# Optimization experiments

Hardware: AMD Instinct MI355X
Metric: run time of the kernel (lower is better)

Reference implementation:

```python
import jax, jax.numpy as jnp
import numpy as np

STRIDES = (8, 16, 32, 64, 128)
SIZES = (128, 64, 32, 16, 8)
B, C = 16, 80
K = 1000            # pre_nms_max_boxes
THRESHOLD = 0.05    # detection confidence threshold
NMS_THR = 0.5
PAD = -1.0


def setup_inputs() -> dict:
    key = jax.random.key(0)
    ks = jax.random.split(key, 15)
    inp = {}
    for i, (s, hw) in enumerate(zip(STRIDES, SIZES)):
        inp[f"cls{i}"] = jax.random.normal(ks[3 * i], (B, C, hw, hw), jnp.float32)
        # reg is post-ReLU (non-negative) distances; scale by stride for realistic extents
        inp[f"reg{i}"] = jax.random.uniform(ks[3 * i + 1], (B, 4, hw, hw), jnp.float32) * (2.0 * s)
        inp[f"ctr{i}"] = jax.random.normal(ks[3 * i + 2], (B, 1, hw, hw), jnp.float32)
    return inp


def _decode_level(cls_l, ctr_l, reg_l, stride):
    # cls_l: [B,C,H,W] logits, ctr_l: [B,1,H,W] logits, reg_l: [B,4,H,W] (l,t,r,b)
    b, c, h, w = cls_l.shape
    p = jax.nn.sigmoid(cls_l)
    cen = jax.nn.sigmoid(ctr_l)
    scaled = jnp.sqrt(p * cen)  # sqrt(cls * centerness), broadcast over C
    ys = jnp.arange(h, dtype=cls_l.dtype) * stride + stride / 2.0
    xs = jnp.arange(w, dtype=cls_l.dtype) * stride + stride / 2.0
    cx = jnp.broadcast_to(xs[None, :], (h, w))
    cy = jnp.broadcast_to(ys[:, None], (h, w))
    l, t, r, bt = reg_l[:, 0], reg_l[:, 1], reg_l[:, 2], reg_l[:, 3]  # [B,H,W]
    boxes = jnp.stack([cx - l, cy - t, cx + r, cy + bt], axis=-1)  # [B,H,W,4]
    return p.reshape(b, c, h * w), scaled.reshape(b, c, h * w), boxes.reshape(b, h * w, 4)


def _iou_matrix(boxes):
    # boxes: [K,4] -> [K,K] IoU
    x1, y1, x2, y2 = boxes[:, 0], boxes[:, 1], boxes[:, 2], boxes[:, 3]
    area = jnp.clip(x2 - x1, 0.0) * jnp.clip(y2 - y1, 0.0)
    ix1 = jnp.maximum(x1[:, None], x1[None, :])
    iy1 = jnp.maximum(y1[:, None], y1[None, :])
    ix2 = jnp.minimum(x2[:, None], x2[None, :])
    iy2 = jnp.minimum(y2[:, None], y2[None, :])
    inter = jnp.clip(ix2 - ix1, 0.0) * jnp.clip(iy2 - iy1, 0.0)
    union = area[:, None] + area[None, :] - inter
    return inter / jnp.maximum(union, 1e-9)


def _nms_one(boxes, cls_id, valid):
    # greedy class-aware NMS on score-descending boxes; returns keep mask [K]
    iou = _iou_matrix(boxes)
    same = cls_id[:, None] == cls_id[None, :]  # batched_nms: only same class suppresses
    sup = (iou > NMS_THR) & same
    rng = jnp.arange(boxes.shape[0])
    def body(i, keep):
        s = sup[i] & (rng > i) & keep[i]
        return keep & (~s)
    return jax.lax.fori_loop(0, boxes.shape[0], body, valid)


def reference(cls0, cls1, cls2, cls3, cls4,
              reg0, reg1, reg2, reg3, reg4,
              ctr0, ctr1, ctr2, ctr3, ctr4):
    cls_levels = (cls0, cls1, cls2, cls3, cls4)
    reg_levels = (reg0, reg1, reg2, reg3, reg4)
    ctr_levels = (ctr0, ctr1, ctr2, ctr3, ctr4)
    raws, scaleds, boxes_list = [], [], []
    for cl, ct, rg, s in zip(cls_levels, ctr_levels, reg_levels, STRIDES):
        r, sc, bx = _decode_level(cl, ct, rg, s)
        raws.append(r); scaleds.append(sc); boxes_list.append(bx)
    raw = jnp.concatenate(raws, axis=-1)        # [B,C,L]
    scaled = jnp.concatenate(scaleds, axis=-1)  # [B,C,L]
    boxes = jnp.concatenate(boxes_list, axis=1) # [B,L,4]
    b, c, L = raw.shape
    valid = raw >= THRESHOLD  # threshold on raw cls probability
    masked = jnp.where(valid, scaled, -1.0).reshape(b, c * L)
    topv, topi = jax.lax.top_k(masked, K)  # per-batch pre-NMS limit, sorted desc by scaled score
    cls_id = topi // L
    loc = topi % L
    boxes_k = jnp.take_along_axis(boxes, loc[..., None], axis=1)  # [B,K,4]
    scaled_k = jnp.take_along_axis(scaled.reshape(b, c * L), topi, axis=1)  # [B,K]
    valid_k = topv >= 0.0
    keep = jax.vmap(_nms_one)(boxes_k, cls_id, valid_k)  # [B,K]
    out = jnp.concatenate(
        [boxes_k, scaled_k[..., None], cls_id.astype(boxes_k.dtype)[..., None]], axis=-1)  # [B,K,6]
    return jnp.where(keep[..., None], out, PAD)
```

## Files before the change

kernel.cpp:

```cpp
#include <hip/hip_runtime.h>
#include <stdint.h>

typedef uint32_t u32;
typedef uint64_t u64;
typedef unsigned short u16;

#define NB 16
#define NC 80
#define LTOT 21824
#define TOPK 1000
#define CAP2 6144
#define NBINS 1024
#define KEYSH 12
#define BINBASE 0x3F580u
#define T2SQ 0.7119140625f
#define PACKS8 2728
#define CGRP 20
#define NSHARD 8
#define PSH 4096
#define SSTAGE 512

struct P5 { const float* a; const float* b; const float* c; const float* d; const float* e; };

__device__ __forceinline__ const float* selp(const P5& p, int lvl) {
    const float* q = p.a;
    if (lvl == 1) q = p.b;
    else if (lvl == 2) q = p.c;
    else if (lvl == 3) q = p.d;
    else if (lvl == 4) q = p.e;
    return q;
}

__device__ __forceinline__ void locate(int loc, int& lvl, int& off) {
    if (loc < 16384)      { lvl = 0; off = 0; }
    else if (loc < 20480) { lvl = 1; off = 16384; }
    else if (loc < 21504) { lvl = 2; off = 20480; }
    else if (loc < 21760) { lvl = 3; off = 21504; }
    else                  { lvl = 4; off = 21760; }
}

__device__ __forceinline__ void locate_pack8(int pk, int& lvl, int& poff, int& loff) {
    if (pk < 2048)      { lvl = 0; poff = 0;    loff = 0; }
    else if (pk < 2560) { lvl = 1; poff = 2048; loff = 16384; }
    else if (pk < 2688) { lvl = 2; poff = 2560; loff = 20480; }
    else if (pk < 2720) { lvl = 3; poff = 2688; loff = 21504; }
    else                { lvl = 4; poff = 2720; loff = 21760; }
}

__device__ __forceinline__ float sigmoidf_(float x) {
    return 1.0f / (1.0f + expf(-x));
}

__global__ __launch_bounds__(256) void k_ctr(P5 ctr, float* __restrict__ cen, float* __restrict__ Larr,
                                             u32* __restrict__ hist, u32* __restrict__ pcnt,
                                             float* __restrict__ out) {
    int tid = threadIdx.x;
    int b = blockIdx.y;
    if (blockIdx.x == 0) {
        for (int i = tid; i < NBINS; i += 256) hist[b * NBINS + i] = 0;
        if (tid < NSHARD * 16) pcnt[b * NSHARD * 16 + tid] = 0;
    }
    {
        int oi = blockIdx.x * 256 + tid;
        if (oi < TOPK * 6) out[b * TOPK * 6 + oi] = -1.0f;
    }
    int loc = blockIdx.x * 256 + tid;
    if (loc >= LTOT) return;
    int lvl, off; locate(loc, lvl, off);
    int d = loc - off;
    int hw = 1 << (2 * (7 - lvl));
    float x = selp(ctr, lvl)[b * hw + d];
    float cv = sigmoidf_(x);
    float L;
    float q = T2SQ / cv;
    if (!(q < 1.0f)) {
        L = 3.0e38f;
    } else {
        float qm = q * 0.999996f;
        L = logf(qm / (1.0f - qm)) - 1.0e-3f;
    }
    cen[b * LTOT + loc] = cv;
    Larr[b * LTOT + loc] = L;
}

__global__ __launch_bounds__(256, 8) void k_sweep(P5 cls, const float* __restrict__ Larr,
                                                  const float* __restrict__ cen,
                                                  u32* __restrict__ hist, u32* __restrict__ pcnt,
                                                  u64* __restrict__ pcand) {
    __shared__ u32 lh[NBINS];
    __shared__ u64 stage[SSTAGE];
    __shared__ u64 outk[SSTAGE];
    __shared__ u32 scnt, ocnt, sbase;
    int tid = threadIdx.x;
    for (int i = tid; i < NBINS; i += 256) lh[i] = 0;
    if (tid == 0) { scnt = 0; ocnt = 0; }
    __syncthreads();

    int b  = blockIdx.z;
    int cg = blockIdx.y;
    int pk = blockIdx.x * 256 + tid;
    int shard = (blockIdx.x + blockIdx.y) & (NSHARD - 1);
    u32* pc = &pcnt[(b * NSHARD + shard) * 16];
    u64* pdst = pcand + (size_t)(b * NSHARD + shard) * PSH;

    if (pk < PACKS8) {
        int lvl, poff, loff; locate_pack8(pk, lvl, poff, loff);
        int d0 = (pk - poff) * 8;
        int hw = 1 << (2 * (7 - lvl));
        int gl = b * LTOT + loff + d0;
        int loc0 = loff + d0;
        float4 La = *(const float4*)&Larr[gl];
        float4 Lb = *(const float4*)&Larr[gl + 4];
        const float* base = selp(cls, lvl) + ((size_t)(b * NC + cg * 4)) * hw + d0;

        float4 Av[4], Bv[4];
        #pragma unroll
        for (int i = 0; i < 4; ++i) {
            Av[i] = *(const float4*)(base + (size_t)i * hw);
            Bv[i] = *(const float4*)(base + (size_t)i * hw + 4);
        }

        #pragma unroll
        for (int i = 0; i < 4; ++i) {
            float4 a0 = Av[i], b0 = Bv[i];
            bool any = (a0.x >= La.x) | (a0.y >= La.y) | (a0.z >= La.z) | (a0.w >= La.w)
                     | (b0.x >= Lb.x) | (b0.y >= Lb.y) | (b0.z >= Lb.z) | (b0.w >= Lb.w);
            if (any) {
                u32 c = (u32)(cg * 4 + i);
#define ELEM(X, LV, J) \
                if ((X) >= (LV)) { \
                    u32 p = atomicAdd(&scnt, 1u); \
                    u64 ent = ((u64)__float_as_uint(X) << 32) | (u64)((c << 15) | (u32)(loc0 + (J))); \
                    if (p < SSTAGE) stage[p] = ent; \
                    else {  \
                        float cv = cen[gl + (J)]; \
                        float sv = sqrtf(sigmoidf_(X) * cv); \
                        u32 bits = __float_as_uint(sv); \
                        u32 key = bits >> KEYSH; \
                        if (key >= BINBASE) { \
                            atomicAdd(&lh[min(key - BINBASE, (u32)(NBINS - 1))], 1u); \
                            u32 q2 = atomicAdd(pc, 1u); \
                            if (q2 < PSH) pdst[q2] = ((u64)bits << 32) | (u32)(~(c * (u32)LTOT + (u32)(loc0 + (J)))); \
                        } \
                    } \
                }
                ELEM(a0.x, La.x, 0) ELEM(a0.y, La.y, 1) ELEM(a0.z, La.z, 2) ELEM(a0.w, La.w, 3)
                ELEM(b0.x, Lb.x, 4) ELEM(b0.y, Lb.y, 5) ELEM(b0.z, Lb.z, 6) ELEM(b0.w, Lb.w, 7)
#undef ELEM
            }
        }
    }
    __syncthreads();

    u32 m2 = scnt; if (m2 > SSTAGE) m2 = SSTAGE;
    for (u32 i = tid; i < m2; i += 256) {
        u64 e = stage[i];
        u32 xbits = (u32)(e >> 32);
        u32 eid   = (u32)e;
        u32 c     = eid >> 15;
        u32 loc   = eid & 0x7FFFu;
        float X  = __uint_as_float(xbits);
        float cv = cen[b * LTOT + loc];
        float sv = sqrtf(sigmoidf_(X) * cv);
        u32 bits = __float_as_uint(sv);
        u32 key = bits >> KEYSH;
        if (key >= BINBASE) {
            atomicAdd(&lh[min(key - BINBASE, (u32)(NBINS - 1))], 1u);
            u32 p = atomicAdd(&ocnt, 1u);
            outk[p] = ((u64)bits << 32) | (u32)(~(c * (u32)LTOT + loc));
        }
    }
    __syncthreads();

    for (u32 i = tid; i < NBINS; i += 256) {
        u32 v = lh[i];
        if (v) atomicAdd(&hist[b * NBINS + i], v);
    }
    u32 m3 = ocnt; if (m3 > SSTAGE) m3 = SSTAGE;
    if (tid == 0 && m3) sbase = atomicAdd(pc, m3);
    __syncthreads();
    for (u32 i = tid; i < m3; i += 256) {
        u32 q = sbase + i;
        if (q < PSH) pdst[q] = outk[i];
    }
}

__global__ __launch_bounds__(1024) void k_rank(const u64* __restrict__ pcand, const u32* __restrict__ pcnt,
                                               const u32* __restrict__ hist, u32* __restrict__ cnt,
                                               P5 reg, float* __restrict__ boxesWs,
                                               float* __restrict__ scoreWs, int* __restrict__ clsWs) {
    __shared__ u64 sh[CAP2];
    __shared__ u32 tot[NBINS];
    __shared__ u32 sufL[NBINS];
    __shared__ u32 bcnt[NBINS];
    __shared__ u32 wtot[16];
    __shared__ u32 cbase[NSHARD + 1];
    __shared__ u32 thrT;
    int b = blockIdx.x, tid = threadIdx.x;
    int lane = tid & 63, w = tid >> 6;

    u32 v = hist[b * NBINS + tid];
    tot[tid] = v;
    bcnt[tid] = 0;
    if (tid < NSHARD) {
        u32 c0 = pcnt[(b * NSHARD + tid) * 16];
        cbase[tid] = (c0 > (u32)PSH) ? (u32)PSH : c0;
    }
    if (tid == 0) thrT = 0;

    u32 s = v;
    #pragma unroll
    for (int d2 = 1; d2 < 64; d2 <<= 1) {
        u32 t = (u32)__shfl_down((int)s, d2, 64);
        if (lane + d2 < 64) s += t;
    }
    if (lane == 0) wtot[w] = s;
    __syncthreads();

    u32 add = 0;
    #pragma unroll
    for (int w2 = 0; w2 < 16; ++w2) if (w2 > w) add += wtot[w2];
    s += add;
    sufL[tid] = s;
    if (tid == 0) {
        u32 acc = 0;
        #pragma unroll
        for (int i = 0; i < NSHARD; ++i) { u32 t = cbase[i]; cbase[i] = acc; acc += t; }
        cbase[NSHARD] = acc;
    }
    __syncthreads();

    {
        u32 sv = sufL[tid];
        u32 snext = (tid + 1 < NBINS) ? sufL[tid + 1] : 0;
        if (sv >= (u32)TOPK && snext < (u32)TOPK) thrT = (u32)tid;
    }
    __syncthreads();
    u32 T = thrT;
    u32 tb = BINBASE + T;
    u32 totc = cbase[NSHARD];

    for (u32 idx = tid; idx < totc; idx += 1024) {
        int sg = 0;
        #pragma unroll
        for (int i = 1; i < NSHARD; ++i) sg += (idx >= cbase[i]);
        u32 i2 = idx - cbase[sg];
        u64 key = pcand[(size_t)(b * NSHARD + sg) * PSH + i2];
        u32 kb = (u32)(key >> (32 + KEYSH));
        if (kb >= tb) {
            u32 bin = min(kb - BINBASE, (u32)(NBINS - 1));
            u32 pos = (sufL[bin] - tot[bin]) + atomicAdd(&bcnt[bin], 1u);
            if (pos < CAP2) sh[pos] = key;
        }
    }
    __syncthreads();
    u32 n = sufL[T]; if (n > CAP2) n = CAP2;
    if (tid == 0) cnt[b * 16] = (n > (u32)TOPK) ? (u32)TOPK : n;

    for (u32 e = tid; e < n; e += 1024) {
        u64 key = sh[e];
        u32 bin = min((u32)(key >> (32 + KEYSH)) - BINBASE, (u32)(NBINS - 1));
        u32 s0 = sufL[bin] - tot[bin];
        u32 s1 = sufL[bin]; if (s1 > n) s1 = n;
        u32 r = s0;
        for (u32 i2 = s0; i2 < s1; ++i2) r += (sh[i2] > key);
        if (r < TOPK) {
            u32 bits = (u32)(key >> 32);
            u32 idx  = ~((u32)key);
            int c   = (int)(idx / (u32)LTOT);
            int loc = (int)(idx - (u32)c * (u32)LTOT);
            int lvl, off; locate(loc, lvl, off);
            int d = loc - off;
            int logw = 7 - lvl;
            int ww = 1 << logw, hw = ww * ww;
            int y = d >> logw, x = d & (ww - 1);
            const float* rp = selp(reg, lvl);
            int base = (b * 4) * hw + d;
            float lf = rp[base], tf = rp[base + hw], rf = rp[base + 2 * hw], bf = rp[base + 3 * hw];
            int stride = 8 << lvl;
            float cx = (float)(x * stride) + 0.5f * (float)stride;
            float cy = (float)(y * stride) + 0.5f * (float)stride;
            int o = b * TOPK + (int)r;
            boxesWs[o * 4 + 0] = cx - lf; boxesWs[o * 4 + 1] = cy - tf;
            boxesWs[o * 4 + 2] = cx + rf; boxesWs[o * 4 + 3] = cy + bf;
            scoreWs[o] = __uint_as_float(bits); clsWs[o] = c;
        }
    }
}

__global__ __launch_bounds__(64) void k_nms(const float* __restrict__ boxesWs, const float* __restrict__ scoreWs,
                                            const int* __restrict__ clsWs, const u32* __restrict__ cnt,
                                            float* __restrict__ out) {
    __shared__ u16 list[TOPK];
    __shared__ u32 keptW[32];
    int c = blockIdx.x, b = blockIdx.y;
    int lane = threadIdx.x;
    int n = (int)cnt[b * 16]; if (n > TOPK) n = TOPK;

    int m = 0;
    for (int k0 = 0; k0 < n; k0 += 64) {
        int j = k0 + lane;
        int cj = (j < n) ? clsWs[b * TOPK + j] : -2;
        u64 mask = __ballot(cj == c);
        int pos = m + __popcll(mask & ((lane == 0) ? 0ull : (~0ull >> (64 - lane))));
        if (cj == c) list[pos] = (u16)j;
        m += (int)__popcll(mask);
    }
    __syncthreads();
    if (m == 0) return;

    if (m <= 64) {
        int j = (lane < m) ? (int)list[lane] : (int)list[0];
        float4 bx = ((const float4*)boxesWs)[b * TOPK + j];
        float ar = fmaxf(bx.z - bx.x, 0.f) * fmaxf(bx.w - bx.y, 0.f);
        u64 kept = (m < 64) ? ((1ull << m) - 1ull) : ~0ull;
        u64 todo = kept;
        while (todo) {
            int i = __builtin_ctzll(todo);
            todo &= todo - 1;
            float bix = __shfl(bx.x, i, 64);
            float biy = __shfl(bx.y, i, 64);
            float biz = __shfl(bx.z, i, 64);
            float biw = __shfl(bx.w, i, 64);
            float ai  = __shfl(ar,   i, 64);
            float ix1 = fmaxf(bix, bx.x), iy1 = fmaxf(biy, bx.y);
            float ix2 = fminf(biz, bx.z), iy2 = fminf(biw, bx.w);
            float inter = fmaxf(ix2 - ix1, 0.f) * fmaxf(iy2 - iy1, 0.f);
            float uni = fmaxf(ai + ar - inter, 1e-9f);
            float iou = inter / uni;
            u64 sup = __ballot(lane > i && lane < m && iou > 0.5f);
            kept &= ~sup;
            todo &= ~sup;
        }
        if (lane < m && ((kept >> lane) & 1ull)) {
            int o = b * TOPK + j;
            float sc = scoreWs[o];
            out[o * 6 + 0] = bx.x; out[o * 6 + 1] = bx.y; out[o * 6 + 2] = bx.z;
            out[o * 6 + 3] = bx.w; out[o * 6 + 4] = sc;   out[o * 6 + 5] = (float)c;
        }
    } else {
        if (lane < 32) keptW[lane] = 0;
        __syncthreads();
        for (int i = lane; i < m; i += 64) atomicOr(&keptW[i >> 5], 1u << (i & 31));
        __syncthreads();
        for (int i = 0; i < m; ++i) {
            if (!((keptW[i >> 5] >> (i & 31)) & 1u)) { __syncthreads(); continue; }
            int ji = (int)list[i];
            float4 bi = ((const float4*)boxesWs)[b * TOPK + ji];
            float ai = fmaxf(bi.z - bi.x, 0.f) * fmaxf(bi.w - bi.y, 0.f);
            for (int jj = i + 1 + lane; jj < m; jj += 64) {
                int j2 = (int)list[jj];
                float4 bj = ((const float4*)boxesWs)[b * TOPK + j2];
                float aj = fmaxf(bj.z - bj.x, 0.f) * fmaxf(bj.w - bj.y, 0.f);
                float ix1 = fmaxf(bi.x, bj.x), iy1 = fmaxf(bi.y, bj.y);
                float ix2 = fminf(bi.z, bj.z), iy2 = fminf(bi.w, bj.w);
                float inter = fmaxf(ix2 - ix1, 0.f) * fmaxf(iy2 - iy1, 0.f);
                float uni = fmaxf(ai + aj - inter, 1e-9f);
                if (inter / uni > 0.5f) atomicAnd(&keptW[jj >> 5], ~(1u << (jj & 31)));
            }
            __syncthreads();
        }
        for (int i = lane; i < m; i += 64) {
            if ((keptW[i >> 5] >> (i & 31)) & 1u) {
                int j2 = (int)list[i];
                int o = b * TOPK + j2;
                float4 bj = ((const float4*)boxesWs)[o];
                float sc = scoreWs[o];
                out[o * 6 + 0] = bj.x; out[o * 6 + 1] = bj.y; out[o * 6 + 2] = bj.z;
                out[o * 6 + 3] = bj.w; out[o * 6 + 4] = sc;   out[o * 6 + 5] = (float)c;
            }
        }
    }
}

extern "C" void kernel_launch(void* const* d_in, const int* in_sizes, int n_in,
                              void* d_out, int out_size, void* d_ws, size_t ws_size,
                              hipStream_t stream) {
    const float* cls[5]; const float* reg[5]; const float* ctr[5];
    for (int i = 0; i < 5; ++i) {
        cls[i] = (const float*)d_in[3 * i + 0];
        reg[i] = (const float*)d_in[3 * i + 1];
        ctr[i] = (const float*)d_in[3 * i + 2];
    }
    P5 Pc = { cls[0], cls[1], cls[2], cls[3], cls[4] };
    P5 Pr = { reg[0], reg[1], reg[2], reg[3], reg[4] };
    P5 Pt = { ctr[0], ctr[1], ctr[2], ctr[3], ctr[4] };

    char* ws = (char*)d_ws;
    u32*   hist    = (u32*)(ws + 0);
    u32*   pcnt    = (u32*)(ws + 131072);
    u32*   cnt     = (u32*)(ws + 196608);
    float* cen     = (float*)(ws + 262144);
    float* Larr    = (float*)(ws + 1703936);
    u64*   pcand   = (u64*)(ws + 3145728);
    float* boxesWs = (float*)(ws + 7864320);
    float* scoreWs = (float*)(ws + 8388608);
    int*   clsWs   = (int*)(ws + 8519680);

    k_ctr<<<dim3((LTOT + 255) / 256, NB), 256, 0, stream>>>(Pt, cen, Larr, hist, pcnt, (float*)d_out);
    dim3 sweep((PACKS8 + 255) / 256, CGRP, NB);
    k_sweep<<<sweep, 256, 0, stream>>>(Pc, Larr, cen, hist, pcnt, pcand);
    k_rank<<<NB, 1024, 0, stream>>>(pcand, pcnt, hist, cnt, Pr, boxesWs, scoreWs, clsWs);
    k_nms<<<dim3(NC, NB), 64, 0, stream>>>(boxesWs, scoreWs, clsWs, cnt, (float*)d_out);
}
```

Before: 59.46 us.

## Fuse centerness into sweep and merge rank with per-class NMS

The separate centerness kernel goes away: each sweep thread now loads the centerness logits and computes the screening threshold and sigmoid inline, and the zeroing of histogram and counters moves to a memset. The rank and NMS kernels are merged into one block per batch, with boxes, scores and classes kept in shared memory and each of 16 waves handling 5 classes in turn. Every output slot is written exactly once, either as a box or as padding. This removes two launches and the global round-trips through the workspace, at the cost of recomputing sigmoid/log per class group, and it serialises NMS into 16 blocks with one wave per class instead of 1280 blocks.

```diff
diff --git a/kernel.cpp b/kernel.cpp
--- a/kernel.cpp
+++ b/kernel.cpp
@@ -51,44 +51,19 @@
     return 1.0f / (1.0f + expf(-x));
 }
 
-__global__ __launch_bounds__(256) void k_ctr(P5 ctr, float* __restrict__ cen, float* __restrict__ Larr,
-                                             u32* __restrict__ hist, u32* __restrict__ pcnt,
-                                             float* __restrict__ out) {
-    int tid = threadIdx.x;
-    int b = blockIdx.y;
-    if (blockIdx.x == 0) {
-        for (int i = tid; i < NBINS; i += 256) hist[b * NBINS + i] = 0;
-        if (tid < NSHARD * 16) pcnt[b * NSHARD * 16 + tid] = 0;
-    }
-    {
-        int oi = blockIdx.x * 256 + tid;
-        if (oi < TOPK * 6) out[b * TOPK * 6 + oi] = -1.0f;
-    }
-    int loc = blockIdx.x * 256 + tid;
-    if (loc >= LTOT) return;
-    int lvl, off; locate(loc, lvl, off);
-    int d = loc - off;
-    int hw = 1 << (2 * (7 - lvl));
-    float x = selp(ctr, lvl)[b * hw + d];
+__device__ __forceinline__ float screenL(float x) {
     float cv = sigmoidf_(x);
-    float L;
     float q = T2SQ / cv;
-    if (!(q < 1.0f)) {
-        L = 3.0e38f;
-    } else {
-        float qm = q * 0.999996f;
-        L = logf(qm / (1.0f - qm)) - 1.0e-3f;
-    }
-    cen[b * LTOT + loc] = cv;
-    Larr[b * LTOT + loc] = L;
-}
-
-__global__ __launch_bounds__(256, 8) void k_sweep(P5 cls, const float* __restrict__ Larr,
-                                                  const float* __restrict__ cen,
+    if (!(q < 1.0f)) return 3.0e38f;
+    float qm = q * 0.999996f;
+    return logf(qm / (1.0f - qm)) - 1.0e-3f;
+}
+
+__global__ __launch_bounds__(256, 8) void k_sweep(P5 cls, P5 ctr,
                                                   u32* __restrict__ hist, u32* __restrict__ pcnt,
                                                   u64* __restrict__ pcand) {
     __shared__ u32 lh[NBINS];
-    __shared__ u64 stage[SSTAGE];
+    __shared__ u64 stageA[SSTAGE];
     __shared__ u64 outk[SSTAGE];
     __shared__ u32 scnt, ocnt, sbase;
     int tid = threadIdx.x;
@@ -107,10 +82,8 @@
         int lvl, poff, loff; locate_pack8(pk, lvl, poff, loff);
         int d0 = (pk - poff) * 8;
         int hw = 1 << (2 * (7 - lvl));
-        int gl = b * LTOT + loff + d0;
         int loc0 = loff + d0;
-        float4 La = *(const float4*)&Larr[gl];
-        float4 Lb = *(const float4*)&Larr[gl + 4];
+        const float* tpp  = selp(ctr, lvl) + (size_t)b * hw + d0;
         const float* base = selp(cls, lvl) + ((size_t)(b * NC + cg * 4)) * hw + d0;
 
         float4 Av[4], Bv[4];
@@ -119,6 +92,12 @@
             Av[i] = *(const float4*)(base + (size_t)i * hw);
             Bv[i] = *(const float4*)(base + (size_t)i * hw + 4);
         }
+        float4 t0 = *(const float4*)tpp;
+        float4 t1 = *(const float4*)(tpp + 4);
+
+        float4 La, Lb;
+        La.x = screenL(t0.x); La.y = screenL(t0.y); La.z = screenL(t0.z); La.w = screenL(t0.w);
+        Lb.x = screenL(t1.x); Lb.y = screenL(t1.y); Lb.z = screenL(t1.z); Lb.w = screenL(t1.w);
 
         #pragma unroll
         for (int i = 0; i < 4; ++i) {
@@ -131,9 +110,10 @@
                 if ((X) >= (LV)) { \
                     u32 p = atomicAdd(&scnt, 1u); \
                     u64 ent = ((u64)__float_as_uint(X) << 32) | (u64)((c << 15) | (u32)(loc0 + (J))); \
-                    if (p < SSTAGE) stage[p] = ent; \
+                    if (p < SSTAGE) stageA[p] = ent; \
                     else {  \
-                        float cv = cen[gl + (J)]; \
+                        float xv = tpp[(J)]; \
+                        float cv = sigmoidf_(xv); \
                         float sv = sqrtf(sigmoidf_(X) * cv); \
                         u32 bits = __float_as_uint(sv); \
                         u32 key = bits >> KEYSH; \
@@ -154,14 +134,17 @@
 
     u32 m2 = scnt; if (m2 > SSTAGE) m2 = SSTAGE;
     for (u32 i = tid; i < m2; i += 256) {
-        u64 e = stage[i];
+        u64 e = stageA[i];
         u32 xbits = (u32)(e >> 32);
         u32 eid   = (u32)e;
         u32 c     = eid >> 15;
         u32 loc   = eid & 0x7FFFu;
-        float X  = __uint_as_float(xbits);
-        float cv = cen[b * LTOT + loc];
-        float sv = sqrtf(sigmoidf_(X) * cv);
+        int lvl, off; locate((int)loc, lvl, off);
+        int d = (int)loc - off;
+        int hw = 1 << (2 * (7 - lvl));
+        float xv = selp(ctr, lvl)[(size_t)b * hw + d];
+        float cv = sigmoidf_(xv);
+        float sv = sqrtf(sigmoidf_(__uint_as_float(xbits)) * cv);
         u32 bits = __float_as_uint(sv);
         u32 key = bits >> KEYSH;
         if (key >= BINBASE) {
@@ -185,10 +168,9 @@
     }
 }
 
-__global__ __launch_bounds__(1024) void k_rank(const u64* __restrict__ pcand, const u32* __restrict__ pcnt,
-                                               const u32* __restrict__ hist, u32* __restrict__ cnt,
-                                               P5 reg, float* __restrict__ boxesWs,
-                                               float* __restrict__ scoreWs, int* __restrict__ clsWs) {
+__global__ __launch_bounds__(1024) void k_ranknms(const u64* __restrict__ pcand, const u32* __restrict__ pcnt,
+                                                  const u32* __restrict__ hist, P5 reg,
+                                                  float* __restrict__ out) {
     __shared__ u64 sh[CAP2];
     __shared__ u32 tot[NBINS];
     __shared__ u32 sufL[NBINS];
@@ -196,6 +178,11 @@
     __shared__ u32 wtot[16];
     __shared__ u32 cbase[NSHARD + 1];
     __shared__ u32 thrT;
+    __shared__ float4 boxL[TOPK];
+    __shared__ float  scL[TOPK];
+    __shared__ u16    clL[TOPK];
+    __shared__ u32    keptW[16][32];
+
     int b = blockIdx.x, tid = threadIdx.x;
     int lane = tid & 63, w = tid >> 6;
 
@@ -255,7 +242,7 @@
     }
     __syncthreads();
     u32 n = sufL[T]; if (n > CAP2) n = CAP2;
-    if (tid == 0) cnt[b * 16] = (n > (u32)TOPK) ? (u32)TOPK : n;
+    u32 Keff = (n > (u32)TOPK) ? (u32)TOPK : n;
 
     for (u32 e = tid; e < n; e += 1024) {
         u64 key = sh[e];
@@ -280,94 +267,98 @@
             int stride = 8 << lvl;
             float cx = (float)(x * stride) + 0.5f * (float)stride;
             float cy = (float)(y * stride) + 0.5f * (float)stride;
-            int o = b * TOPK + (int)r;
-            boxesWs[o * 4 + 0] = cx - lf; boxesWs[o * 4 + 1] = cy - tf;
-            boxesWs[o * 4 + 2] = cx + rf; boxesWs[o * 4 + 3] = cy + bf;
-            scoreWs[o] = __uint_as_float(bits); clsWs[o] = c;
-        }
-    }
-}
-
-__global__ __launch_bounds__(64) void k_nms(const float* __restrict__ boxesWs, const float* __restrict__ scoreWs,
-                                            const int* __restrict__ clsWs, const u32* __restrict__ cnt,
-                                            float* __restrict__ out) {
-    __shared__ u16 list[TOPK];
-    __shared__ u32 keptW[32];
-    int c = blockIdx.x, b = blockIdx.y;
-    int lane = threadIdx.x;
-    int n = (int)cnt[b * 16]; if (n > TOPK) n = TOPK;
-
-    int m = 0;
-    for (int k0 = 0; k0 < n; k0 += 64) {
-        int j = k0 + lane;
-        int cj = (j < n) ? clsWs[b * TOPK + j] : -2;
-        u64 mask = __ballot(cj == c);
-        int pos = m + __popcll(mask & ((lane == 0) ? 0ull : (~0ull >> (64 - lane))));
-        if (cj == c) list[pos] = (u16)j;
-        m += (int)__popcll(mask);
-    }
-    __syncthreads();
-    if (m == 0) return;
-
-    if (m <= 64) {
-        int j = (lane < m) ? (int)list[lane] : (int)list[0];
-        float4 bx = ((const float4*)boxesWs)[b * TOPK + j];
-        float ar = fmaxf(bx.z - bx.x, 0.f) * fmaxf(bx.w - bx.y, 0.f);
-        u64 kept = (m < 64) ? ((1ull << m) - 1ull) : ~0ull;
-        u64 todo = kept;
-        while (todo) {
-            int i = __builtin_ctzll(todo);
-            todo &= todo - 1;
-            float bix = __shfl(bx.x, i, 64);
-            float biy = __shfl(bx.y, i, 64);
-            float biz = __shfl(bx.z, i, 64);
-            float biw = __shfl(bx.w, i, 64);
-            float ai  = __shfl(ar,   i, 64);
-            float ix1 = fmaxf(bix, bx.x), iy1 = fmaxf(biy, bx.y);
-            float ix2 = fminf(biz, bx.z), iy2 = fminf(biw, bx.w);
-            float inter = fmaxf(ix2 - ix1, 0.f) * fmaxf(iy2 - iy1, 0.f);
-            float uni = fmaxf(ai + ar - inter, 1e-9f);
-            float iou = inter / uni;
-            u64 sup = __ballot(lane > i && lane < m && iou > 0.5f);
-            kept &= ~sup;
-            todo &= ~sup;
-        }
-        if (lane < m && ((kept >> lane) & 1ull)) {
-            int o = b * TOPK + j;
-            float sc = scoreWs[o];
-            out[o * 6 + 0] = bx.x; out[o * 6 + 1] = bx.y; out[o * 6 + 2] = bx.z;
-            out[o * 6 + 3] = bx.w; out[o * 6 + 4] = sc;   out[o * 6 + 5] = (float)c;
-        }
-    } else {
-        if (lane < 32) keptW[lane] = 0;
-        __syncthreads();
-        for (int i = lane; i < m; i += 64) atomicOr(&keptW[i >> 5], 1u << (i & 31));
-        __syncthreads();
-        for (int i = 0; i < m; ++i) {
-            if (!((keptW[i >> 5] >> (i & 31)) & 1u)) { __syncthreads(); continue; }
-            int ji = (int)list[i];
-            float4 bi = ((const float4*)boxesWs)[b * TOPK + ji];
-            float ai = fmaxf(bi.z - bi.x, 0.f) * fmaxf(bi.w - bi.y, 0.f);
-            for (int jj = i + 1 + lane; jj < m; jj += 64) {
-                int j2 = (int)list[jj];
-                float4 bj = ((const float4*)boxesWs)[b * TOPK + j2];
-                float aj = fmaxf(bj.z - bj.x, 0.f) * fmaxf(bj.w - bj.y, 0.f);
-                float ix1 = fmaxf(bi.x, bj.x), iy1 = fmaxf(bi.y, bj.y);
-                float ix2 = fminf(bi.z, bj.z), iy2 = fminf(bi.w, bj.w);
+            float4 bx; bx.x = cx - lf; bx.y = cy - tf; bx.z = cx + rf; bx.w = cy + bf;
+            boxL[r] = bx;
+            scL[r] = __uint_as_float(bits);
+            clL[r] = (u16)c;
+        }
+    }
+    for (u32 j = Keff + tid; j < (u32)TOPK; j += 1024) {
+        int o = b * TOPK + (int)j;
+        #pragma unroll
+        for (int q2 = 0; q2 < 6; ++q2) out[o * 6 + q2] = -1.0f;
+    }
+    __syncthreads();
+
+    u16* list = ((u16*)sh) + (size_t)w * 1024;
+    for (int k5 = 0; k5 < 5; ++k5) {
+        int c = w + (k5 << 4);
+        int m = 0;
+        for (int k0 = 0; k0 < (int)Keff; k0 += 64) {
+            int j = k0 + lane;
+            int cj = (j < (int)Keff) ? (int)clL[j] : -2;
+            u64 mask = __ballot(cj == c);
+            u64 ltm = (lane == 0) ? 0ull : (~0ull >> (64 - lane));
+            int pos = m + (int)__popcll(mask & ltm);
+            if (cj == c) list[pos] = (u16)j;
+            m += (int)__popcll(mask);
+        }
+        if (m == 0) continue;
+
+        if (m <= 64) {
+            int j = (lane < m) ? (int)list[lane] : (int)list[0];
+            float4 bx = boxL[j];
+            float ar = fmaxf(bx.z - bx.x, 0.f) * fmaxf(bx.w - bx.y, 0.f);
+            u64 kept = (m < 64) ? ((1ull << m) - 1ull) : ~0ull;
+            u64 todo = kept;
+            while (todo) {
+                int i = __builtin_ctzll(todo);
+                todo &= todo - 1;
+                float bix = __shfl(bx.x, i, 64);
+                float biy = __shfl(bx.y, i, 64);
+                float biz = __shfl(bx.z, i, 64);
+                float biw = __shfl(bx.w, i, 64);
+                float ai  = __shfl(ar,   i, 64);
+                float ix1 = fmaxf(bix, bx.x), iy1 = fmaxf(biy, bx.y);
+                float ix2 = fminf(biz, bx.z), iy2 = fminf(biw, bx.w);
                 float inter = fmaxf(ix2 - ix1, 0.f) * fmaxf(iy2 - iy1, 0.f);
-                float uni = fmaxf(ai + aj - inter, 1e-9f);
-                if (inter / uni > 0.5f) atomicAnd(&keptW[jj >> 5], ~(1u << (jj & 31)));
-            }
-            __syncthreads();
-        }
-        for (int i = lane; i < m; i += 64) {
-            if ((keptW[i >> 5] >> (i & 31)) & 1u) {
+                float uni = fmaxf(ai + ar - inter, 1e-9f);
+                float iou = inter / uni;
+                u64 sup = __ballot(lane > i && lane < m && iou > 0.5f);
+                kept &= ~sup;
+                todo &= ~sup;
+            }
+            if (lane < m) {
+                int o = b * TOPK + j;
+                if ((kept >> lane) & 1ull) {
+                    out[o * 6 + 0] = bx.x; out[o * 6 + 1] = bx.y; out[o * 6 + 2] = bx.z;
+                    out[o * 6 + 3] = bx.w; out[o * 6 + 4] = scL[j]; out[o * 6 + 5] = (float)c;
+                } else {
+                    #pragma unroll
+                    for (int q2 = 0; q2 < 6; ++q2) out[o * 6 + q2] = -1.0f;
+                }
+            }
+        } else {
+            u32* kw = keptW[w];
+            if (lane < 32) kw[lane] = 0;
+            for (int i = lane; i < m; i += 64) atomicOr(&kw[i >> 5], 1u << (i & 31));
+            for (int i = 0; i < m; ++i) {
+                if (!((kw[i >> 5] >> (i & 31)) & 1u)) continue;
+                int ji = (int)list[i];
+                float4 bi = boxL[ji];
+                float ai = fmaxf(bi.z - bi.x, 0.f) * fmaxf(bi.w - bi.y, 0.f);
+                for (int jj = i + 1 + lane; jj < m; jj += 64) {
+                    int j2 = (int)list[jj];
+                    float4 bj = boxL[j2];
+                    float aj = fmaxf(bj.z - bj.x, 0.f) * fmaxf(bj.w - bj.y, 0.f);
+                    float ix1 = fmaxf(bi.x, bj.x), iy1 = fmaxf(bi.y, bj.y);
+                    float ix2 = fminf(bi.z, bj.z), iy2 = fminf(bi.w, bj.w);
+                    float inter = fmaxf(ix2 - ix1, 0.f) * fmaxf(iy2 - iy1, 0.f);
+                    float uni = fmaxf(ai + aj - inter, 1e-9f);
+                    if (inter / uni > 0.5f) atomicAnd(&kw[jj >> 5], ~(1u << (jj & 31)));
+                }
+            }
+            for (int i = lane; i < m; i += 64) {
                 int j2 = (int)list[i];
                 int o = b * TOPK + j2;
-                float4 bj = ((const float4*)boxesWs)[o];
-                float sc = scoreWs[o];
-                out[o * 6 + 0] = bj.x; out[o * 6 + 1] = bj.y; out[o * 6 + 2] = bj.z;
-                out[o * 6 + 3] = bj.w; out[o * 6 + 4] = sc;   out[o * 6 + 5] = (float)c;
+                if ((kw[i >> 5] >> (i & 31)) & 1u) {
+                    float4 bj = boxL[j2];
+                    out[o * 6 + 0] = bj.x; out[o * 6 + 1] = bj.y; out[o * 6 + 2] = bj.z;
+                    out[o * 6 + 3] = bj.w; out[o * 6 + 4] = scL[j2]; out[o * 6 + 5] = (float)c;
+                } else {
+                    #pragma unroll
+                    for (int q2 = 0; q2 < 6; ++q2) out[o * 6 + q2] = -1.0f;
+                }
             }
         }
     }
@@ -388,18 +379,12 @@
 
     char* ws = (char*)d_ws;
     u32*   hist    = (u32*)(ws + 0);
-    u32*   pcnt    = (u32*)(ws + 131072);
-    u32*   cnt     = (u32*)(ws + 196608);
-    float* cen     = (float*)(ws + 262144);
-    float* Larr    = (float*)(ws + 1703936);
-    u64*   pcand   = (u64*)(ws + 3145728);
-    float* boxesWs = (float*)(ws + 7864320);
-    float* scoreWs = (float*)(ws + 8388608);
-    int*   clsWs   = (int*)(ws + 8519680);
-
-    k_ctr<<<dim3((LTOT + 255) / 256, NB), 256, 0, stream>>>(Pt, cen, Larr, hist, pcnt, (float*)d_out);
+    u32*   pcnt    = (u32*)(ws + 65536);
+    u64*   pcand   = (u64*)(ws + 131072);
+
+    hipMemsetAsync(ws, 0, 65536 + NB * NSHARD * 16 * sizeof(u32), stream);
+
     dim3 sweep((PACKS8 + 255) / 256, CGRP, NB);
-    k_sweep<<<sweep, 256, 0, stream>>>(Pc, Larr, cen, hist, pcnt, pcand);
-    k_rank<<<NB, 1024, 0, stream>>>(pcand, pcnt, hist, cnt, Pr, boxesWs, scoreWs, clsWs);
-    k_nms<<<dim3(NC, NB), 64, 0, stream>>>(boxesWs, scoreWs, clsWs, cnt, (float*)d_out);
-}
+    k_sweep<<<sweep, 256, 0, stream>>>(Pc, Pt, hist, pcnt, pcand);
+    k_ranknms<<<NB, 1024, 0, stream>>>(pcand, pcnt, hist, Pr, (float*)d_out);
+}
```

After: 77.28 us. 30.0% more time.
